# Kernel tuning notes

Hardware: AMD Instinct MI355X
Metric: run time of the kernel (lower is better)

The kernel has to match this reference:

```python
import jax, jax.numpy as jnp
import numpy as np

N = 50000        # nodes
E = 1600000      # edges (before self-loops)
HID = 128
HEADS = 4
HD = HID // HEADS
FIN = 32 + 7     # node feats + scenario feats
EPS = 1e-5


def _ln(x, g, b):
    m = x.mean(-1, keepdims=True)
    v = ((x - m) ** 2).mean(-1, keepdims=True)
    return (x - m) / jnp.sqrt(v + EPS) * g + b


def _gat(x, src, dst, W, a_s, a_d, bias):
    # PyG GATConv (concat=True, negative_slope=0.2), eval mode (no dropout)
    xp = (x @ W).reshape(-1, HEADS, HD)                    # [N,H,C]
    es = (xp * a_s).sum(-1)                                # [N,H]
    ed = (xp * a_d).sum(-1)                                # [N,H]
    e = jax.nn.leaky_relu(es[src] + ed[dst], 0.2)          # [Etot,H]
    emax = jax.ops.segment_max(e, dst, num_segments=N)     # per-target softmax (self-loops guarantee nonempty segments)
    a = jnp.exp(e - emax[dst])
    denom = jax.ops.segment_sum(a, dst, num_segments=N)
    a = a / denom[dst]
    out = jax.ops.segment_sum(xp[src] * a[:, :, None], dst, num_segments=N)
    return out.reshape(-1, HID) + bias


def setup_inputs() -> dict:
    key = jax.random.key(0)
    ks = iter(jax.random.split(key, 64))

    def rn(shape, scale=0.05):
        return jax.random.normal(next(ks), shape, dtype=jnp.float32) * scale

    inp = {}
    inp["x"] = jax.random.normal(next(ks), (N, FIN), dtype=jnp.float32)
    inp["edge_index"] = jax.random.randint(next(ks), (2, E), 0, N)
    inp["enc_w1"] = rn((FIN, HID)); inp["enc_b1"] = jnp.zeros((HID,), jnp.float32)
    inp["enc_w2"] = rn((HID, HID)); inp["enc_b2"] = jnp.zeros((HID,), jnp.float32)
    for l in (1, 2, 3):
        inp[f"W{l}"] = rn((HID, HID))
        inp[f"as{l}"] = rn((HEADS, HD))
        inp[f"ad{l}"] = rn((HEADS, HD))
        inp[f"bc{l}"] = jnp.zeros((HID,), jnp.float32)
        inp[f"g{l}"] = jnp.ones((HID,), jnp.float32)
        inp[f"be{l}"] = jnp.zeros((HID,), jnp.float32)
    inp["imp_w1"] = rn((HID, HID // 2)); inp["imp_b1"] = jnp.zeros((HID // 2,), jnp.float32)
    inp["imp_w2"] = rn((HID // 2, 3));   inp["imp_b2"] = jnp.zeros((3,), jnp.float32)
    inp["tim_w1"] = rn((HID, HID // 2)); inp["tim_b1"] = jnp.zeros((HID // 2,), jnp.float32)
    inp["tim_w2"] = rn((HID // 2, 2));   inp["tim_b2"] = jnp.zeros((2,), jnp.float32)
    return inp


def reference(x, edge_index, enc_w1, enc_b1, enc_w2, enc_b2,
              W1, as1, ad1, bc1, g1, be1,
              W2, as2, ad2, bc2, g2, be2,
              W3, as3, ad3, bc3, g3, be3,
              imp_w1, imp_b1, imp_w2, imp_b2,
              tim_w1, tim_b1, tim_w2, tim_b2):
    loops = jnp.arange(N, dtype=edge_index.dtype)          # add_self_loops=True
    src = jnp.concatenate([edge_index[0], loops])
    dst = jnp.concatenate([edge_index[1], loops])
    h = jax.nn.relu(x @ enc_w1 + enc_b1) @ enc_w2 + enc_b2
    for (W, a_s, a_d, bc, g, be) in ((W1, as1, ad1, bc1, g1, be1),
                                     (W2, as2, ad2, bc2, g2, be2),
                                     (W3, as3, ad3, bc3, g3, be3)):
        h = jax.nn.relu(_ln(_gat(h, src, dst, W, a_s, a_d, bc) + h, g, be))
    impact = jax.nn.relu(h @ imp_w1 + imp_b1) @ imp_w2 + imp_b2
    timing = jax.nn.softplus(jax.nn.relu(h @ tim_w1 + tim_b1) @ tim_w2 + tim_b2)
    return (impact, timing)
```

## Files before the change

### kernel.cpp

```cpp
#include <hip/hip_runtime.h>
#include <hip/hip_bf16.h>
#include <math.h>

#define NN 50000
#define EDGES 1600000
#define ETOT (EDGES + NN)
#define FINDIM 39
#define NPART 256
#define PSZ 196
#define PCAP 7100
#define P1TILE 4096

__device__ __forceinline__ unsigned pack_bf16(float a, float b) {
    __hip_bfloat162 t;
    t.x = __float2bfloat16(a);
    t.y = __float2bfloat16(b);
    return *(unsigned*)&t;
}
__device__ __forceinline__ float2 unpack_bf16(unsigned w) {
    float2 r;
    r.x = __uint_as_float(w << 16);
    r.y = __uint_as_float(w & 0xffff0000u);
    return r;
}

__device__ __forceinline__ int src_at(const int* ei, int i, bool i32) {
    return i32 ? ei[i] : ei[2 * i];
}
__device__ __forceinline__ int dst_at(const int* ei, int i, bool i32) {
    return i32 ? ei[EDGES + i] : ei[2 * (EDGES + i)];
}

__global__ __launch_bounds__(256) void pass1_kernel(const int* __restrict__ ei,
                                                    int* __restrict__ gcursor,
                                                    unsigned* __restrict__ pbuf) {
    __shared__ unsigned raw[P1TILE];
    __shared__ unsigned srt[P1TILE];
    __shared__ int pcnt[NPART], poff[NPART], pcur[NPART], gb[NPART];
    __shared__ int i32flag;
    int t = threadIdx.x;
    if (t == 0) i32flag = 0;
    __syncthreads();
    int chunk = (ETOT + gridDim.x - 1) / gridDim.x;
    int c0 = blockIdx.x * chunk;
    int c1 = c0 + chunk; if (c1 > ETOT) c1 = ETOT;
    int sb = c0 < EDGES - 64 ? c0 : 0;
    if (t < 64 && ei[2 * (sb + t) + 1] != 0) i32flag = 1;
    __syncthreads();
    bool i32 = (i32flag != 0);
    for (int t0 = c0; t0 < c1; t0 += P1TILE) {
        int tn = c1 - t0; if (tn > P1TILE) tn = P1TILE;
        pcnt[t] = 0; pcur[t] = 0;
        __syncthreads();
        for (int i = t; i < tn; i += 256) {
            int e = t0 + i;
            int s, d;
            if (e < EDGES) { s = src_at(ei, e, i32); d = dst_at(ei, e, i32); }
            else { s = d = e - EDGES; }
            raw[i] = ((unsigned)s << 16) | (unsigned)d;
            atomicAdd(&pcnt[d / PSZ], 1);
        }
        __syncthreads();
        poff[t] = pcnt[t];
        __syncthreads();
        for (int off = 1; off < NPART; off <<= 1) {
            int v = (t >= off) ? poff[t - off] : 0;
            __syncthreads();
            poff[t] += v;
            __syncthreads();
        }
        poff[t] -= pcnt[t];
        gb[t] = atomicAdd(&gcursor[t], pcnt[t]);
        __syncthreads();
        for (int i = t; i < tn; i += 256) {
            unsigned r = raw[i];
            int part = (int)(r & 0xFFFFu) / PSZ;
            int pos = poff[part] + atomicAdd(&pcur[part], 1);
            srt[pos] = r;
        }
        __syncthreads();
        for (int i = t; i < tn; i += 256) {
            unsigned r = srt[i];
            int part = (int)(r & 0xFFFFu) / PSZ;
            int gpos = gb[part] + (i - poff[part]);
            if (gpos < PCAP) pbuf[(size_t)part * PCAP + gpos] = r;
        }
        __syncthreads();
    }
}

__global__ __launch_bounds__(256) void pass2_kernel(const unsigned* __restrict__ pbuf,
                                                    const int* __restrict__ gcursor,
                                                    int* __restrict__ rowptr,
                                                    int* __restrict__ colidx) {
    __shared__ unsigned recs[PCAP];
    __shared__ int lhist[PSZ], lexcl[PSZ], lcur[PSZ];
    __shared__ int psm[NPART];
    int p = blockIdx.x;
    int t = threadIdx.x;
    psm[t] = gcursor[t];
    __syncthreads();
    for (int off = 1; off < NPART; off <<= 1) {
        int x = (t >= off) ? psm[t - off] : 0;
        __syncthreads();
        psm[t] += x;
        __syncthreads();
    }
    int n = gcursor[p]; if (n > PCAP) n = PCAP;
    int base = psm[p] - gcursor[p];
    if (p == NPART - 1 && t == 0) rowptr[NN] = psm[NPART - 1];
    int d0 = p * PSZ;
    int nd = NN - d0; if (nd > PSZ) nd = PSZ;
    if (nd < 0) nd = 0;
    for (int i = t; i < nd; i += 256) { lhist[i] = 0; lcur[i] = 0; }
    __syncthreads();
    for (int i = t; i < n; i += 256) {
        unsigned r = pbuf[(size_t)p * PCAP + i];
        recs[i] = r;
        atomicAdd(&lhist[(int)(r & 0xFFFFu) - d0], 1);
    }
    __syncthreads();
    for (int i = t; i < nd; i += 256) lexcl[i] = lhist[i];
    __syncthreads();
    for (int off = 1; off < PSZ; off <<= 1) {
        int a0 = 0;
        if (t < nd && t >= off) a0 = lexcl[t - off];
        __syncthreads();
        if (t < nd) lexcl[t] += a0;
        __syncthreads();
    }
    for (int i = t; i < nd; i += 256) {
        lexcl[i] -= lhist[i];
        rowptr[d0 + i] = base + lexcl[i];
    }
    __syncthreads();
    for (int i = t; i < n; i += 256) {
        unsigned r = recs[i];
        int li = (int)(r & 0xFFFFu) - d0;
        int pos = base + lexcl[li] + atomicAdd(&lcur[li], 1);
        colidx[pos] = (int)(r >> 16);
    }
}

template <int NC, bool RELU>
__global__ __launch_bounds__(256) void gemm_small_kernel(const float* __restrict__ A,
                                                         const float* __restrict__ B,
                                                         const float* __restrict__ bias,
                                                         float* __restrict__ C, int M, int K) {
    constexpr int TM = 32;
    constexpr int GROUPS = 256 / NC;
    constexpr int RPG = TM / GROUPS;
    constexpr int KC = 64;
    __shared__ float As[TM * 128];
    __shared__ float Bs[KC * NC];
    int t = threadIdx.x;
    int i0 = blockIdx.x * TM;

    int rows = M - i0; if (rows > TM) rows = TM;
    for (int idx = t; idx < rows * K; idx += 256) {
        int r = idx / K, k = idx - r * K;
        As[r * K + k] = A[(size_t)(i0 + r) * K + k];
    }

    int col = t % NC, grp = t / NC;
    int rg0 = grp * RPG;
    float acc[RPG];
#pragma unroll
    for (int r = 0; r < RPG; ++r) acc[r] = 0.f;

    for (int k0 = 0; k0 < K; k0 += KC) {
        int kc = K - k0; if (kc > KC) kc = KC;
        __syncthreads();
        for (int idx = t; idx < kc * NC; idx += 256) Bs[idx] = B[(size_t)k0 * NC + idx];
        __syncthreads();
        for (int k = 0; k < kc; ++k) {
            float bv = Bs[k * NC + col];
#pragma unroll
            for (int r = 0; r < RPG; ++r) acc[r] += As[(rg0 + r) * K + k0 + k] * bv;
        }
    }

    float bb = bias ? bias[col] : 0.f;
#pragma unroll
    for (int r = 0; r < RPG; ++r) {
        int i = i0 + rg0 + r;
        if (i < M) {
            float v = acc[r] + bb;
            if (RELU) v = v > 0.f ? v : 0.f;
            C[(size_t)i * NC + col] = v;
        }
    }
}

template <bool BIAS, bool EPI>
__global__ __launch_bounds__(256) void gemm128_kernel(const float* __restrict__ A,
                                                      const float* __restrict__ B,
                                                      const float* __restrict__ bias,
                                                      float* __restrict__ C,
                                                      unsigned* __restrict__ XP,
                                                      const float* __restrict__ a_s,
                                                      const float* __restrict__ a_d,
                                                      float* __restrict__ es,
                                                      float* __restrict__ ed, int M) {
    __shared__ float As[64 * 32];
    __shared__ float Bs[32 * 128];
    int t = threadIdx.x;
    int i0 = blockIdx.x * 64;
    int tc = t & 31;
    int tr = t >> 5;
    int r0 = tr * 8;
    int c0 = tc * 4;

    float acc[8][4];
#pragma unroll
    for (int i = 0; i < 8; ++i)
#pragma unroll
        for (int j = 0; j < 4; ++j) acc[i][j] = 0.f;

    for (int k0 = 0; k0 < 128; k0 += 32) {
        __syncthreads();
#pragma unroll
        for (int q = 0; q < 2; ++q) {
            int idx = t + q * 256;
            int r = idx >> 3, kq = idx & 7;
            float4 v4 = make_float4(0.f, 0.f, 0.f, 0.f);
            if (i0 + r < M) v4 = *(const float4*)&A[(size_t)(i0 + r) * 128 + k0 + kq * 4];
            *(float4*)&As[r * 32 + kq * 4] = v4;
        }
#pragma unroll
        for (int q = 0; q < 4; ++q) {
            int idx = (t + q * 256) * 4;
            *(float4*)&Bs[idx] = *(const float4*)&B[(size_t)k0 * 128 + idx];
        }
        __syncthreads();
#pragma unroll 8
        for (int k = 0; k < 32; k += 4) {
            float4 a4[8];
#pragma unroll
            for (int i = 0; i < 8; ++i)
                a4[i] = *(const float4*)&As[(r0 + i) * 32 + k];
            float4 b4[4];
#pragma unroll
            for (int kk = 0; kk < 4; ++kk)
                b4[kk] = *(const float4*)&Bs[(k + kk) * 128 + c0];
#pragma unroll
            for (int i = 0; i < 8; ++i) {
                const float* av = (const float*)&a4[i];
#pragma unroll
                for (int kk = 0; kk < 4; ++kk) {
                    acc[i][0] += av[kk] * b4[kk].x;
                    acc[i][1] += av[kk] * b4[kk].y;
                    acc[i][2] += av[kk] * b4[kk].z;
                    acc[i][3] += av[kk] * b4[kk].w;
                }
            }
        }
    }

    if (!EPI) {
        float4 bias4 = make_float4(0.f, 0.f, 0.f, 0.f);
        if (BIAS) bias4 = *(const float4*)&bias[c0];
#pragma unroll
        for (int i = 0; i < 8; ++i) {
            int row = i0 + r0 + i;
            if (row < M) {
                float4 o;
                o.x = acc[i][0] + bias4.x;
                o.y = acc[i][1] + bias4.y;
                o.z = acc[i][2] + bias4.z;
                o.w = acc[i][3] + bias4.w;
                *(float4*)&C[(size_t)row * 128 + c0] = o;
            }
        }
    } else {
#pragma unroll
        for (int i = 0; i < 8; ++i) {
            int row = i0 + r0 + i;
            if (row < M) {
                uint2 o;
                o.x = pack_bf16(acc[i][0], acc[i][1]);
                o.y = pack_bf16(acc[i][2], acc[i][3]);
                *(uint2*)&XP[(size_t)row * 64 + tc * 2] = o;
            }
        }
        int hd = tc >> 3;
        float4 s4 = *(const float4*)&a_s[c0];
        float4 d4 = *(const float4*)&a_d[c0];
#pragma unroll
        for (int i = 0; i < 8; ++i) {
            int row = i0 + r0 + i;
            float s = acc[i][0] * s4.x + acc[i][1] * s4.y + acc[i][2] * s4.z + acc[i][3] * s4.w;
            float d = acc[i][0] * d4.x + acc[i][1] * d4.y + acc[i][2] * d4.z + acc[i][3] * d4.w;
#pragma unroll
            for (int off = 4; off >= 1; off >>= 1) {
                s += __shfl_xor(s, off);
                d += __shfl_xor(d, off);
            }
            if ((tc & 7) == 0 && row < M) {
                es[row * 4 + hd] = s;
                ed[row * 4 + hd] = d;
            }
        }
    }
}

__global__ __launch_bounds__(256) void gemm_heads_kernel(const float* __restrict__ A,
                                                         const float* __restrict__ iw1,
                                                         const float* __restrict__ ib1,
                                                         const float* __restrict__ tw1,
                                                         const float* __restrict__ tb1,
                                                         const float* __restrict__ iw2,
                                                         const float* __restrict__ ib2,
                                                         const float* __restrict__ tw2,
                                                         const float* __restrict__ tb2,
                                                         float* __restrict__ out, int M) {
    __shared__ float As[64 * 32];
    __shared__ float Bs[32 * 128];
    int t = threadIdx.x;
    int i0 = blockIdx.x * 64;
    int tc = t & 31;
    int tr = t >> 5;
    int r0 = tr * 8;
    int c0 = tc * 4;

    float acc[8][4];
#pragma unroll
    for (int i = 0; i < 8; ++i)
#pragma unroll
        for (int j = 0; j < 4; ++j) acc[i][j] = 0.f;

    for (int k0 = 0; k0 < 128; k0 += 32) {
        __syncthreads();
#pragma unroll
        for (int q = 0; q < 2; ++q) {
            int idx = t + q * 256;
            int r = idx >> 3, kq = idx & 7;
            float4 v4 = make_float4(0.f, 0.f, 0.f, 0.f);
            if (i0 + r < M) v4 = *(const float4*)&A[(size_t)(i0 + r) * 128 + k0 + kq * 4];
            *(float4*)&As[r * 32 + kq * 4] = v4;
        }
#pragma unroll
        for (int q = 0; q < 4; ++q) {
            int idx = (t + q * 256) * 4;
            int k = idx >> 7, cl = idx & 127;
            float4 v4 = (cl < 64)
                ? *(const float4*)&iw1[(size_t)(k0 + k) * 64 + cl]
                : *(const float4*)&tw1[(size_t)(k0 + k) * 64 + (cl - 64)];
            *(float4*)&Bs[idx] = v4;
        }
        __syncthreads();
#pragma unroll 8
        for (int k = 0; k < 32; k += 4) {
            float4 a4[8];
#pragma unroll
            for (int i = 0; i < 8; ++i)
                a4[i] = *(const float4*)&As[(r0 + i) * 32 + k];
            float4 b4[4];
#pragma unroll
            for (int kk = 0; kk < 4; ++kk)
                b4[kk] = *(const float4*)&Bs[(k + kk) * 128 + c0];
#pragma unroll
            for (int i = 0; i < 8; ++i) {
                const float* av = (const float*)&a4[i];
#pragma unroll
                for (int kk = 0; kk < 4; ++kk) {
                    acc[i][0] += av[kk] * b4[kk].x;
                    acc[i][1] += av[kk] * b4[kk].y;
                    acc[i][2] += av[kk] * b4[kk].z;
                    acc[i][3] += av[kk] * b4[kk].w;
                }
            }
        }
    }

    bool isimp = (tc < 16);
    int lc = isimp ? c0 : (c0 - 64);
    float v[8][4];
#pragma unroll
    for (int i = 0; i < 8; ++i)
#pragma unroll
        for (int j = 0; j < 4; ++j) {
            float b = isimp ? ib1[lc + j] : tb1[lc + j];
            float x = acc[i][j] + b;
            v[i][j] = x > 0.f ? x : 0.f;
        }
#pragma unroll
    for (int i = 0; i < 8; ++i) {
        int row = i0 + r0 + i;
        if (isimp) {
#pragma unroll
            for (int c = 0; c < 3; ++c) {
                float pc = v[i][0] * iw2[(lc + 0) * 3 + c] + v[i][1] * iw2[(lc + 1) * 3 + c]
                         + v[i][2] * iw2[(lc + 2) * 3 + c] + v[i][3] * iw2[(lc + 3) * 3 + c];
#pragma unroll
                for (int off = 8; off >= 1; off >>= 1) pc += __shfl_xor(pc, off);
                if (tc == 0 && row < M) out[(size_t)row * 3 + c] = pc + ib2[c];
            }
        } else {
#pragma unroll
            for (int d = 0; d < 2; ++d) {
                float pd = v[i][0] * tw2[(lc + 0) * 2 + d] + v[i][1] * tw2[(lc + 1) * 2 + d]
                         + v[i][2] * tw2[(lc + 2) * 2 + d] + v[i][3] * tw2[(lc + 3) * 2 + d];
#pragma unroll
                for (int off = 8; off >= 1; off >>= 1) pd += __shfl_xor(pd, off);
                if (tc == 16 && row < M) {
                    float a = pd + tb2[d];
                    float sp = a > 20.f ? a : log1pf(__expf(a));
                    out[(size_t)(NN * 3) + (size_t)row * 2 + d] = sp;
                }
            }
        }
    }
}

__global__ __launch_bounds__(256) void gat_kernel(const unsigned* __restrict__ xpk,
                                                  const float* __restrict__ es,
                                                  const float* __restrict__ ed,
                                                  const int* __restrict__ rowptr,
                                                  const int* __restrict__ colidx,
                                                  float* __restrict__ h,
                                                  const float* __restrict__ bc,
                                                  const float* __restrict__ g,
                                                  const float* __restrict__ be) {
    int wv = threadIdx.x >> 6, l = threadIdx.x & 63;
    int v = blockIdx.x * 4 + wv;
    if (v >= NN) return;
    int s0 = rowptr[v], s1 = rowptr[v + 1];
    int hd = l >> 4;
    float edv = ed[(unsigned)(v << 2) + hd];
    float ax = 0.f, ay = 0.f, den = 0.f;
    int p = s0;
    for (; p + 8 <= s1; p += 8) {
        int u[8];
#pragma unroll
        for (int q = 0; q < 8; ++q) u[q] = colidx[p + q];
        unsigned xw[8];
#pragma unroll
        for (int q = 0; q < 8; ++q) xw[q] = xpk[(unsigned)(u[q] << 6) + l];
        float w[8];
#pragma unroll
        for (int q = 0; q < 8; ++q) {
            float e = es[(unsigned)(u[q] << 2) + hd] + edv;
            e = fmaxf(e, 0.2f * e);
            w[q] = __expf(e);
        }
#pragma unroll
        for (int q = 0; q < 8; ++q) {
            float2 x = unpack_bf16(xw[q]);
            ax = fmaf(w[q], x.x, ax);
            ay = fmaf(w[q], x.y, ay);
            den += w[q];
        }
    }
    for (; p < s1; ++p) {
        int u = colidx[p];
        float e = es[(unsigned)(u << 2) + hd] + edv;
        e = fmaxf(e, 0.2f * e);
        float w = __expf(e);
        float2 x = unpack_bf16(xpk[(unsigned)(u << 6) + l]);
        ax = fmaf(w, x.x, ax);
        ay = fmaf(w, x.y, ay);
        den += w;
    }
    float rd = 1.f / den;

    float2 h2  = *(const float2*)&h[(size_t)v * 128 + 2 * l];
    float2 bc2 = *(const float2*)&bc[2 * l];
    float y0 = ax * rd + bc2.x + h2.x;
    float y1 = ay * rd + bc2.y + h2.y;

    float s = y0 + y1;
#pragma unroll
    for (int off = 32; off >= 1; off >>= 1) s += __shfl_xor(s, off);
    float mean = s * (1.f / 128.f);
    float d0 = y0 - mean, d1 = y1 - mean;
    float vv = d0 * d0 + d1 * d1;
#pragma unroll
    for (int off = 32; off >= 1; off >>= 1) vv += __shfl_xor(vv, off);
    float rstd = rsqrtf(vv * (1.f / 128.f) + 1e-5f);
    float2 g2  = *(const float2*)&g[2 * l];
    float2 be2 = *(const float2*)&be[2 * l];
    float z0 = d0 * rstd * g2.x + be2.x;
    float z1 = d1 * rstd * g2.y + be2.y;
    float2 o;
    o.x = z0 > 0.f ? z0 : 0.f;
    o.y = z1 > 0.f ? z1 : 0.f;
    *(float2*)&h[(size_t)v * 128 + 2 * l] = o;
}

extern "C" void kernel_launch(void* const* d_in, const int* in_sizes, int n_in,
                              void* d_out, int out_size, void* d_ws, size_t ws_size,
                              hipStream_t stream) {
    const float* x      = (const float*)d_in[0];
    const int*   ei     = (const int*)d_in[1];
    const float* enc_w1 = (const float*)d_in[2];
    const float* enc_b1 = (const float*)d_in[3];
    const float* enc_w2 = (const float*)d_in[4];
    const float* enc_b2 = (const float*)d_in[5];
    const float *W[3], *as_[3], *ad_[3], *bc[3], *g[3], *be[3];
    for (int l = 0; l < 3; ++l) {
        W[l]   = (const float*)d_in[6 + l * 6 + 0];
        as_[l] = (const float*)d_in[6 + l * 6 + 1];
        ad_[l] = (const float*)d_in[6 + l * 6 + 2];
        bc[l]  = (const float*)d_in[6 + l * 6 + 3];
        g[l]   = (const float*)d_in[6 + l * 6 + 4];
        be[l]  = (const float*)d_in[6 + l * 6 + 5];
    }
    const float* imp_w1 = (const float*)d_in[24];
    const float* imp_b1 = (const float*)d_in[25];
    const float* imp_w2 = (const float*)d_in[26];
    const float* imp_b2 = (const float*)d_in[27];
    const float* tim_w1 = (const float*)d_in[28];
    const float* tim_b1 = (const float*)d_in[29];
    const float* tim_w2 = (const float*)d_in[30];
    const float* tim_b2 = (const float*)d_in[31];

    int* gcursor = (int*)d_ws;
    int* rowptr  = gcursor + NPART + 64;
    int* colidx  = rowptr + NN + 1;
    uintptr_t pb = (uintptr_t)(colidx + ETOT);
    pb = (pb + 255) & ~(uintptr_t)255;
    unsigned* pbuf = (unsigned*)pb;
    uintptr_t fb = (uintptr_t)(pbuf + (size_t)NPART * PCAP);
    fb = (fb + 255) & ~(uintptr_t)255;
    float* es = (float*)fb;
    float* ed = es + (size_t)NN * 4;
    float* h  = ed + (size_t)NN * 4;
    float* xpf = h + (size_t)NN * 128;
    unsigned* xpk = (unsigned*)xpf;
    float* tmp = xpf;

    hipMemsetAsync(gcursor, 0, NPART * sizeof(int), stream);
    pass1_kernel<<<512, 256, 0, stream>>>(ei, gcursor, pbuf);
    pass2_kernel<<<NPART, 256, 0, stream>>>(pbuf, gcursor, rowptr, colidx);

    const int GB64 = (NN + 63) / 64;
    gemm_small_kernel<128, true><<<(NN + 31) / 32, 256, 0, stream>>>(x, enc_w1, enc_b1, tmp, NN, FINDIM);
    gemm128_kernel<true, false><<<GB64, 256, 0, stream>>>(tmp, enc_w2, enc_b2, h, nullptr,
                                                          nullptr, nullptr, nullptr, nullptr, NN);

    for (int l = 0; l < 3; ++l) {
        gemm128_kernel<false, true><<<GB64, 256, 0, stream>>>(h, W[l], nullptr, nullptr, xpk,
                                                              as_[l], ad_[l], es, ed, NN);
        gat_kernel<<<(NN + 3) / 4, 256, 0, stream>>>(xpk, es, ed, rowptr, colidx, h,
                                                     bc[l], g[l], be[l]);
    }

    gemm_heads_kernel<<<GB64, 256, 0, stream>>>(h, imp_w1, imp_b1, tim_w1, tim_b1,
                                                imp_w2, imp_b2, tim_w2, tim_b2,
                                                (float*)d_out, NN);
}
```

Measured before the change: 565.6 us.

## Compute GAT edge weights once per lane group and share via ds_bpermute

The GAT aggregation now remaps lanes so each lane holds one (edge, head) attention logit for an 8-edge chunk. Each exp is computed once and broadcast to the lanes that need it with ds_bpermute, so the 16 lanes of a head no longer each compute the same exp redundantly. The scalar tail loop is removed by padding colidx with 8 zeroed sentinels and masking weights beyond the row end. The price is extra cross-lane traffic per edge, a lane-to-column remapping, and over-fetching feature rows for masked padding edges.

```diff
diff --git a/kernel.cpp b/kernel.cpp
--- a/kernel.cpp
+++ b/kernel.cpp
@@ -426,46 +426,40 @@
     int v = blockIdx.x * 4 + wv;
     if (v >= NN) return;
     int s0 = rowptr[v], s1 = rowptr[v + 1];
-    int hd = l >> 4;
-    float edv = ed[(unsigned)(v << 2) + hd];
-    float ax = 0.f, ay = 0.f, den = 0.f;
-    int p = s0;
-    for (; p + 8 <= s1; p += 8) {
+    int hq = l & 3;
+    int j = l >> 2;
+    int qlane = (l & 31) >> 2;
+    int xsel = (hq << 4) + j;
+    int wsel = hq << 2;
+    float edv = ed[(unsigned)(v << 2) + hq];
+
+    float ax = 0.f, ay = 0.f, denp = 0.f;
+    for (int p = s0; p < s1; p += 8) {
+        int rr = s1 - p;
         int u[8];
 #pragma unroll
         for (int q = 0; q < 8; ++q) u[q] = colidx[p + q];
-        unsigned xw[8];
-#pragma unroll
-        for (int q = 0; q < 8; ++q) xw[q] = xpk[(unsigned)(u[q] << 6) + l];
-        float w[8];
+        int ul = colidx[p + qlane];
+        float ev = es[((unsigned)ul << 2) + hq] + edv;
+        ev = fmaxf(ev, 0.2f * ev);
+        float w = (qlane < rr) ? __expf(ev) : 0.f;
+        denp += w;
 #pragma unroll
         for (int q = 0; q < 8; ++q) {
-            float e = es[(unsigned)(u[q] << 2) + hd] + edv;
-            e = fmaxf(e, 0.2f * e);
-            w[q] = __expf(e);
-        }
-#pragma unroll
-        for (int q = 0; q < 8; ++q) {
-            float2 x = unpack_bf16(xw[q]);
-            ax = fmaf(w[q], x.x, ax);
-            ay = fmaf(w[q], x.y, ay);
-            den += w[q];
-        }
-    }
-    for (; p < s1; ++p) {
-        int u = colidx[p];
-        float e = es[(unsigned)(u << 2) + hd] + edv;
-        e = fmaxf(e, 0.2f * e);
-        float w = __expf(e);
-        float2 x = unpack_bf16(xpk[(unsigned)(u << 6) + l]);
-        ax = fmaf(w, x.x, ax);
-        ay = fmaf(w, x.y, ay);
-        den += w;
-    }
-    float rd = 1.f / den;
-
-    float2 h2  = *(const float2*)&h[(size_t)v * 128 + 2 * l];
-    float2 bc2 = *(const float2*)&bc[2 * l];
+            float wq = __int_as_float(
+                __builtin_amdgcn_ds_bpermute(wsel + (q << 4), __float_as_int(w)));
+            float2 x = unpack_bf16(xpk[((unsigned)u[q] << 6) + xsel]);
+            ax = fmaf(wq, x.x, ax);
+            ay = fmaf(wq, x.y, ay);
+        }
+    }
+#pragma unroll
+    for (int off = 4; off <= 16; off <<= 1) denp += __shfl_xor(denp, off);
+    float rd = 1.f / denp;
+
+    int c0 = (hq << 5) + (j << 1);
+    float2 h2  = *(const float2*)&h[(size_t)v * 128 + c0];
+    float2 bc2 = *(const float2*)&bc[c0];
     float y0 = ax * rd + bc2.x + h2.x;
     float y1 = ay * rd + bc2.y + h2.y;
 
@@ -478,14 +472,14 @@
 #pragma unroll
     for (int off = 32; off >= 1; off >>= 1) vv += __shfl_xor(vv, off);
     float rstd = rsqrtf(vv * (1.f / 128.f) + 1e-5f);
-    float2 g2  = *(const float2*)&g[2 * l];
-    float2 be2 = *(const float2*)&be[2 * l];
+    float2 g2  = *(const float2*)&g[c0];
+    float2 be2 = *(const float2*)&be[c0];
     float z0 = d0 * rstd * g2.x + be2.x;
     float z1 = d1 * rstd * g2.y + be2.y;
     float2 o;
     o.x = z0 > 0.f ? z0 : 0.f;
     o.y = z1 > 0.f ? z1 : 0.f;
-    *(float2*)&h[(size_t)v * 128 + 2 * l] = o;
+    *(float2*)&h[(size_t)v * 128 + c0] = o;
 }
 
 extern "C" void kernel_launch(void* const* d_in, const int* in_sizes, int n_in,
@@ -518,7 +512,7 @@
     int* gcursor = (int*)d_ws;
     int* rowptr  = gcursor + NPART + 64;
     int* colidx  = rowptr + NN + 1;
-    uintptr_t pb = (uintptr_t)(colidx + ETOT);
+    uintptr_t pb = (uintptr_t)(colidx + ETOT + 8);
     pb = (pb + 255) & ~(uintptr_t)255;
     unsigned* pbuf = (unsigned*)pb;
     uintptr_t fb = (uintptr_t)(pbuf + (size_t)NPART * PCAP);
@@ -531,6 +525,7 @@
     float* tmp = xpf;
 
     hipMemsetAsync(gcursor, 0, NPART * sizeof(int), stream);
+    hipMemsetAsync(colidx + ETOT, 0, 8 * sizeof(int), stream);
     pass1_kernel<<<512, 256, 0, stream>>>(ei, gcursor, pbuf);
     pass2_kernel<<<NPART, 256, 0, stream>>>(pbuf, gcursor, rowptr, colidx);
 
```

Result: slower. 663.9 us (+17.4%).

## Process two nodes per wavefront in GAT aggregation with 8-byte feature gathers

Applied to the files above, without the earlier changes.

The GAT aggregation kernel now maps two destination nodes onto each 64-lane wavefront, 32 lanes per node. Each lane gathers 4 bf16 features as a uint2 instead of 2, which halves the number of gather instructions and the per-edge es loads per node. Both halves of the wave loop up to the longer neighbor list, with indices clamped and weights masked to zero past the end. This removes the scalar tail loop but wastes lanes when the two degrees differ. Launch bounds now request 6 blocks per multiprocessor, and the workspace gets extra padding after colidx.

```diff
diff --git a/kernel.cpp b/kernel.cpp
--- a/kernel.cpp
+++ b/kernel.cpp
@@ -413,79 +413,91 @@
     }
 }
 
-__global__ __launch_bounds__(256) void gat_kernel(const unsigned* __restrict__ xpk,
-                                                  const float* __restrict__ es,
-                                                  const float* __restrict__ ed,
-                                                  const int* __restrict__ rowptr,
-                                                  const int* __restrict__ colidx,
-                                                  float* __restrict__ h,
-                                                  const float* __restrict__ bc,
-                                                  const float* __restrict__ g,
-                                                  const float* __restrict__ be) {
+__global__ __launch_bounds__(256, 6) void gat_kernel(const unsigned* __restrict__ xpk,
+                                                     const float* __restrict__ es,
+                                                     const float* __restrict__ ed,
+                                                     const int* __restrict__ rowptr,
+                                                     const int* __restrict__ colidx,
+                                                     float* __restrict__ h,
+                                                     const float* __restrict__ bc,
+                                                     const float* __restrict__ g,
+                                                     const float* __restrict__ be) {
     int wv = threadIdx.x >> 6, l = threadIdx.x & 63;
-    int v = blockIdx.x * 4 + wv;
+    int hf = l >> 5;
+    int lh = l & 31;
+    int hd = lh >> 3;
+    int j  = lh & 7;
+    int v = blockIdx.x * 8 + wv * 2 + hf;
     if (v >= NN) return;
     int s0 = rowptr[v], s1 = rowptr[v + 1];
-    int hd = l >> 4;
-    float edv = ed[(unsigned)(v << 2) + hd];
-    float ax = 0.f, ay = 0.f, den = 0.f;
-    int p = s0;
-    for (; p + 8 <= s1; p += 8) {
+    int len = s1 - s0;
+    int nmax = max(len, __shfl_xor(len, 32));
+    int c0 = (hd << 5) + (j << 2);
+    int xsel = (hd << 4) + (j << 1);
+    float edv = ed[((unsigned)v << 2) + hd];
+
+    float4 h4 = *(const float4*)&h[(size_t)v * 128 + c0];
+
+    float a0 = 0.f, a1 = 0.f, a2 = 0.f, a3 = 0.f, den = 0.f;
+    for (int p8 = 0; p8 < nmax; p8 += 8) {
         int u[8];
 #pragma unroll
-        for (int q = 0; q < 8; ++q) u[q] = colidx[p + q];
-        unsigned xw[8];
-#pragma unroll
-        for (int q = 0; q < 8; ++q) xw[q] = xpk[(unsigned)(u[q] << 6) + l];
+        for (int q = 0; q < 8; ++q) {
+            int idx = p8 + q;
+            u[q] = colidx[s0 + (idx < len ? idx : len - 1)];
+        }
+        uint2 xw[8];
+#pragma unroll
+        for (int q = 0; q < 8; ++q)
+            xw[q] = *(const uint2*)&xpk[((unsigned)u[q] << 6) + xsel];
         float w[8];
 #pragma unroll
         for (int q = 0; q < 8; ++q) {
-            float e = es[(unsigned)(u[q] << 2) + hd] + edv;
+            float e = es[((unsigned)u[q] << 2) + hd] + edv;
             e = fmaxf(e, 0.2f * e);
-            w[q] = __expf(e);
+            float ww = __expf(e);
+            w[q] = (p8 + q < len) ? ww : 0.f;
+            den += w[q];
         }
 #pragma unroll
         for (int q = 0; q < 8; ++q) {
-            float2 x = unpack_bf16(xw[q]);
-            ax = fmaf(w[q], x.x, ax);
-            ay = fmaf(w[q], x.y, ay);
-            den += w[q];
-        }
-    }
-    for (; p < s1; ++p) {
-        int u = colidx[p];
-        float e = es[(unsigned)(u << 2) + hd] + edv;
-        e = fmaxf(e, 0.2f * e);
-        float w = __expf(e);
-        float2 x = unpack_bf16(xpk[(unsigned)(u << 6) + l]);
-        ax = fmaf(w, x.x, ax);
-        ay = fmaf(w, x.y, ay);
-        den += w;
+            float2 x0 = unpack_bf16(xw[q].x);
+            float2 x1 = unpack_bf16(xw[q].y);
+            a0 = fmaf(w[q], x0.x, a0);
+            a1 = fmaf(w[q], x0.y, a1);
+            a2 = fmaf(w[q], x1.x, a2);
+            a3 = fmaf(w[q], x1.y, a3);
+        }
     }
     float rd = 1.f / den;
 
-    float2 h2  = *(const float2*)&h[(size_t)v * 128 + 2 * l];
-    float2 bc2 = *(const float2*)&bc[2 * l];
-    float y0 = ax * rd + bc2.x + h2.x;
-    float y1 = ay * rd + bc2.y + h2.y;
-
-    float s = y0 + y1;
-#pragma unroll
-    for (int off = 32; off >= 1; off >>= 1) s += __shfl_xor(s, off);
+    float4 bc4 = *(const float4*)&bc[c0];
+    float y0 = a0 * rd + bc4.x + h4.x;
+    float y1 = a1 * rd + bc4.y + h4.y;
+    float y2 = a2 * rd + bc4.z + h4.z;
+    float y3 = a3 * rd + bc4.w + h4.w;
+
+    float s = y0 + y1 + y2 + y3;
+#pragma unroll
+    for (int off = 16; off >= 1; off >>= 1) s += __shfl_xor(s, off);
     float mean = s * (1.f / 128.f);
-    float d0 = y0 - mean, d1 = y1 - mean;
-    float vv = d0 * d0 + d1 * d1;
-#pragma unroll
-    for (int off = 32; off >= 1; off >>= 1) vv += __shfl_xor(vv, off);
+    float d0 = y0 - mean, d1 = y1 - mean, d2 = y2 - mean, d3 = y3 - mean;
+    float vv = d0 * d0 + d1 * d1 + d2 * d2 + d3 * d3;
+#pragma unroll
+    for (int off = 16; off >= 1; off >>= 1) vv += __shfl_xor(vv, off);
     float rstd = rsqrtf(vv * (1.f / 128.f) + 1e-5f);
-    float2 g2  = *(const float2*)&g[2 * l];
-    float2 be2 = *(const float2*)&be[2 * l];
-    float z0 = d0 * rstd * g2.x + be2.x;
-    float z1 = d1 * rstd * g2.y + be2.y;
-    float2 o;
+    float4 g4  = *(const float4*)&g[c0];
+    float4 be4 = *(const float4*)&be[c0];
+    float z0 = d0 * rstd * g4.x + be4.x;
+    float z1 = d1 * rstd * g4.y + be4.y;
+    float z2 = d2 * rstd * g4.z + be4.z;
+    float z3 = d3 * rstd * g4.w + be4.w;
+    float4 o;
     o.x = z0 > 0.f ? z0 : 0.f;
     o.y = z1 > 0.f ? z1 : 0.f;
-    *(float2*)&h[(size_t)v * 128 + 2 * l] = o;
+    o.z = z2 > 0.f ? z2 : 0.f;
+    o.w = z3 > 0.f ? z3 : 0.f;
+    *(float4*)&h[(size_t)v * 128 + c0] = o;
 }
 
 extern "C" void kernel_launch(void* const* d_in, const int* in_sizes, int n_in,
@@ -518,7 +530,7 @@
     int* gcursor = (int*)d_ws;
     int* rowptr  = gcursor + NPART + 64;
     int* colidx  = rowptr + NN + 1;
-    uintptr_t pb = (uintptr_t)(colidx + ETOT);
+    uintptr_t pb = (uintptr_t)(colidx + ETOT + 8);
     pb = (pb + 255) & ~(uintptr_t)255;
     unsigned* pbuf = (unsigned*)pb;
     uintptr_t fb = (uintptr_t)(pbuf + (size_t)NPART * PCAP);
@@ -542,7 +554,7 @@
     for (int l = 0; l < 3; ++l) {
         gemm128_kernel<false, true><<<GB64, 256, 0, stream>>>(h, W[l], nullptr, nullptr, xpk,
                                                               as_[l], ad_[l], es, ed, NN);
-        gat_kernel<<<(NN + 3) / 4, 256, 0, stream>>>(xpk, es, ed, rowptr, colidx, h,
+        gat_kernel<<<(NN + 7) / 8, 256, 0, stream>>>(xpk, es, ed, rowptr, colidx, h,
                                                      bc[l], g[l], be[l]);
     }
 
```

Result: no change. 562.5 us (-0.6%).
